# Optimization experiments

Hardware: AMD Instinct MI355X
Metric: run time of the kernel (lower is better)

Reference implementation:

```python
import jax, jax.numpy as jnp
import numpy as np

N_HEAD, D_MODEL, D_K, D_V = 16, 1024, 64, 64
BIAS_WEIGHT = 1.0
NEG = -10000.0


def setup_inputs() -> dict:
    key = jax.random.key(0)
    ks = jax.random.split(key, 9)
    B, L = 2, 2048
    q = jax.random.normal(ks[0], (B, L, D_MODEL), dtype=jnp.float32)
    k = jax.random.normal(ks[1], (B, L, D_MODEL), dtype=jnp.float32)
    v = jax.random.normal(ks[2], (B, L, D_MODEL), dtype=jnp.float32)
    mask = jax.random.randint(ks[3], (B, L, L), 0, 2, dtype=jnp.int32)
    bias = jax.random.normal(ks[4], (B, L, L), dtype=jnp.float32)
    s = 1.0 / np.sqrt(D_MODEL)
    w_qs = jax.random.uniform(ks[5], (D_MODEL, N_HEAD * D_K), jnp.float32, -s, s)
    w_ks = jax.random.uniform(ks[6], (D_MODEL, N_HEAD * D_K), jnp.float32, -s, s)
    w_vs = jax.random.uniform(ks[7], (D_MODEL, N_HEAD * D_V), jnp.float32, -s, s)
    w_fc = jax.random.uniform(ks[8], (N_HEAD * D_V, D_MODEL), jnp.float32, -s, s)
    return {"q": q, "k": k, "v": v, "mask": mask, "bias": bias,
            "w_qs": w_qs, "w_ks": w_ks, "w_vs": w_vs, "w_fc": w_fc}


def reference(q, k, v, mask, bias, w_qs, w_ks, w_vs, w_fc):
    B, Lq, _ = q.shape
    # project and split heads: [B, H, L, d]
    qh = (q @ w_qs).reshape(B, Lq, N_HEAD, D_K).transpose(0, 2, 1, 3)
    kh = (k @ w_ks).reshape(B, k.shape[1], N_HEAD, D_K).transpose(0, 2, 1, 3)
    vh = (v @ w_vs).reshape(B, v.shape[1], N_HEAD, D_V).transpose(0, 2, 1, 3)
    temperature = D_K ** 0.5
    attn = jnp.einsum('bhqd,bhkd->bhqk', qh / temperature, kh)
    attn = attn + bias[:, None, :, :] * BIAS_WEIGHT
    attn = jnp.where(mask[:, None, :, :] == 0, NEG, attn)
    attn = jax.nn.softmax(attn, axis=-1)
    out = jnp.einsum('bhqk,bhkd->bhqd', attn, vh)
    out = out.transpose(0, 2, 1, 3).reshape(B, Lq, N_HEAD * D_V)
    return out @ w_fc
```

## Files before the change

### kernel.cpp

```cpp
#include <hip/hip_runtime.h>
#include <cstddef>

#define DEV static __device__ __forceinline__

typedef float f32x4 __attribute__((ext_vector_type(4)));
typedef __bf16 bf16x8 __attribute__((ext_vector_type(8)));
typedef __bf16 bf16x4v __attribute__((ext_vector_type(4)));
typedef unsigned short u16x8 __attribute__((ext_vector_type(8)));
typedef unsigned short u16x4 __attribute__((ext_vector_type(4)));
typedef unsigned u32x2 __attribute__((ext_vector_type(2)));
typedef unsigned u32x4 __attribute__((ext_vector_type(4)));
typedef _Float16 f16;
typedef _Float16 f16x4 __attribute__((ext_vector_type(4)));

constexpr int BB = 2, LL = 2048, DM = 1024, NH = 16, DK = 64;
constexpr float LOG2E = 1.44269504f;

DEV unsigned short f2bf(float f) {
  unsigned u = __builtin_bit_cast(unsigned, f);
  u += 0x7fffu + ((u >> 16) & 1u);
  return (unsigned short)(u >> 16);
}
DEV u16x4 cvt4(f32x4 v) {
  bf16x4v b = __builtin_convertvector(v, bf16x4v);
  return __builtin_bit_cast(u16x4, b);
}
DEV bf16x8 asbf(u16x8 v) { return __builtin_bit_cast(bf16x8, v); }
DEV f32x4 mfma16(u16x8 a, u16x8 b, f32x4 c) {
  return __builtin_amdgcn_mfma_f32_16x16x32_bf16(asbf(a), asbf(b), c, 0, 0, 0);
}
#if __has_builtin(__builtin_amdgcn_exp2f)
DEV float fexp2(float x) { return __builtin_amdgcn_exp2f(x); }
#else
DEV float fexp2(float x) { return exp2f(x); }
#endif
DEV void swap32(unsigned& a, unsigned& b) {
#if __has_builtin(__builtin_amdgcn_permlane32_swap)
  u32x2 r = __builtin_amdgcn_permlane32_swap(a, b, false, false);
  a = r[0]; b = r[1];
#else
  asm("v_permlane32_swap_b32 %0, %1" : "+v"(a), "+v"(b));
#endif
}
DEV void swap16(unsigned& a, unsigned& b) {
#if __has_builtin(__builtin_amdgcn_permlane16_swap)
  u32x2 r = __builtin_amdgcn_permlane16_swap(a, b, false, false);
  a = r[0]; b = r[1];
#else
  asm("v_permlane16_swap_b32 %0, %1" : "+v"(a), "+v"(b));
#endif
}
DEV void g2lds16(const void* g, void* l) {
  __builtin_amdgcn_global_load_lds(
      (const __attribute__((address_space(1))) unsigned int*)g,
      (__attribute__((address_space(3))) unsigned int*)l, 16, 0, 0);
}

__global__ __launch_bounds__(256) void prep_all(
    const float* __restrict__ w0, const float* __restrict__ w1,
    const float* __restrict__ w2, const float* __restrict__ w3,
    unsigned short* __restrict__ wT, const float* __restrict__ s0,
    const float* __restrict__ s1, const float* __restrict__ s2,
    unsigned short* __restrict__ qkvb) {
  int f = blockIdx.x, t = threadIdx.x;
  if (f < 4096) {
    __shared__ float tile[32][33];
    int z = f >> 10, rem = f & 1023;
    int k0 = (rem >> 5) * 32, n0 = (rem & 31) * 32;
    const float* W = (z == 0) ? w0 : (z == 1) ? w1 : (z == 2) ? w2 : w3;
    unsigned short* out = wT + (size_t)z * DM * DM;
    int tx = t & 31, ty = t >> 5;
#pragma unroll
    for (int p = 0; p < 4; p++)
      tile[ty + 8 * p][tx] = W[(size_t)(k0 + ty + 8 * p) * DM + n0 + tx];
    __syncthreads();
#pragma unroll
    for (int p = 0; p < 4; p++)
      out[(size_t)(n0 + ty + 8 * p) * DM + k0 + tx] = f2bf(tile[tx][ty + 8 * p]);
  } else {
    int f3 = f - 4096;
    int z = f3 >> 11;
    const float* src = (z == 0) ? s0 : (z == 1) ? s1 : s2;
    size_t i = ((size_t)(f3 & 2047) * 256 + t) * 8;
    float4 a = *(const float4*)(src + i);
    float4 b = *(const float4*)(src + i + 4);
    u16x8 o;
    o[0] = f2bf(a.x); o[1] = f2bf(a.y); o[2] = f2bf(a.z); o[3] = f2bf(a.w);
    o[4] = f2bf(b.x); o[5] = f2bf(b.y); o[6] = f2bf(b.z); o[7] = f2bf(b.w);
    *(u16x8*)(qkvb + (size_t)z * (size_t)(BB * LL) * DM + i) = o;
  }
}

template <int KITERS>
DEV void gemm_core(const unsigned short* __restrict__ A,
                   const unsigned short* __restrict__ BT,
                   unsigned short* Al, unsigned short* Bl,
                   int m0, int n0, int k0beg, int t, f32x4 (&acc)[4][4]) {
  int lane = t & 63, c = lane & 15, qd = lane >> 4;
  int w = t >> 6, wm = w >> 1, wn = w & 1;
  int r0 = t >> 3;
  int gsw = (t & 7) ^ (r0 & 7);

#pragma unroll 1
  for (int kk = 0; kk < KITERS; ++kk) {
    int k0 = k0beg + kk * 64;
#pragma unroll
    for (int p = 0; p < 4; ++p) {
      g2lds16(&A[(size_t)(m0 + 32 * p + r0) * DM + k0 + 8 * gsw],
              &Al[p * 2048 + w * 512]);
      g2lds16(&BT[(size_t)(n0 + 32 * p + r0) * DM + k0 + 8 * gsw],
              &Bl[p * 2048 + w * 512]);
    }
    __syncthreads();
#pragma unroll
    for (int ks = 0; ks < 2; ++ks) {
      u16x8 af[4], bfr[4];
#pragma unroll
      for (int mt = 0; mt < 4; ++mt)
        af[mt] = *(const u16x8*)&Al[(64 * wm + 16 * mt + c) * 64 +
                                    (((4 * ks + qd) ^ (c & 7)) << 3)];
#pragma unroll
      for (int nt = 0; nt < 4; ++nt)
        bfr[nt] = *(const u16x8*)&Bl[(64 * wn + 16 * nt + c) * 64 +
                                     (((4 * ks + qd) ^ (c & 7)) << 3)];
#pragma unroll
      for (int mt = 0; mt < 4; ++mt)
#pragma unroll
        for (int nt = 0; nt < 4; ++nt)
          acc[mt][nt] = mfma16(af[mt], bfr[nt], acc[mt][nt]);
    }
    __syncthreads();
  }
}

__global__ __launch_bounds__(256, 3) void proj_gemm(
    const unsigned short* __restrict__ qkvb, const unsigned short* __restrict__ wT,
    unsigned short* __restrict__ qh, unsigned short* __restrict__ kh,
    unsigned short* __restrict__ vT, const int* __restrict__ mask,
    const float* __restrict__ bias, f16* __restrict__ bmf) {
  __shared__ unsigned short Al[128 * 64];
  __shared__ unsigned short Bl[128 * 64];
  int o = blockIdx.x, t = threadIdx.x;
  if (o >= 768) {
    int f2 = o - 768;
    int w = t >> 6, lane = t & 63;
    int bq = f2 >> 5;
    int kt = (f2 & 31) * 4 + w;
    int b = bq >> 7, qt = bq & 127;
    int q = qt * 16 + (lane & 15);
    int k = kt * 16 + (lane >> 4) * 4;
    size_t src = ((size_t)b * LL + q) * LL + k;
    int4 mk = *(const int4*)(mask + src);
    float4 bs = *(const float4*)(bias + src);
    f16x4 oo;
    oo[0] = (f16)((mk.x == 0 ? -10000.f : bs.x) * LOG2E);
    oo[1] = (f16)((mk.y == 0 ? -10000.f : bs.y) * LOG2E);
    oo[2] = (f16)((mk.z == 0 ? -10000.f : bs.z) * LOG2E);
    oo[3] = (f16)((mk.w == 0 ? -10000.f : bs.w) * LOG2E);
    *(f16x4*)(bmf + ((size_t)bq * 128 + kt) * 256 + lane * 4) = oo;
    return;
  }
  int wg = (o & 7) * 96 + (o >> 3);
  int z = wg >> 8, rem = wg & 255;
  int m0 = (rem >> 3) * 128, n0 = (rem & 7) * 128;
  const unsigned short* A = qkvb + (size_t)z * BB * LL * DM;
  const unsigned short* BT = wT + (size_t)z * DM * DM;
  int lane = t & 63, c = lane & 15, qd = lane >> 4;
  int w = t >> 6, wm = w >> 1, wn = w & 1;
  f32x4 acc[4][4] = {};
  gemm_core<DM / 64>(A, BT, Al, Bl, m0, n0, 0, t, acc);

  if (z == 2) {
#pragma unroll
    for (int mt = 0; mt < 4; ++mt)
#pragma unroll
      for (int nt = 0; nt < 4; ++nt) {
        int n = n0 + 64 * wn + 16 * nt + c;
        int h = n >> 6, d = n & 63;
        int m = m0 + 64 * wm + 16 * mt + 4 * qd;
        int b = m >> 11, l = m & 2047;
        *(u16x4*)&vT[(((size_t)b * NH + h) * DK + d) * LL + l] = cvt4(acc[mt][nt]);
      }
  } else {
    unsigned short* Ch = z ? kh : qh;
    float scale = z ? 1.0f : 0.125f * LOG2E;
#pragma unroll
    for (int mt = 0; mt < 4; ++mt)
#pragma unroll
      for (int nt = 0; nt < 4; ++nt) {
        int n = n0 + 64 * wn + 16 * nt + c;
        int h = n >> 6, d = n & 63;
#pragma unroll
        for (int i = 0; i < 4; ++i) {
          int m = m0 + 64 * wm + 16 * mt + 4 * qd + i;
          int b = m >> 11, l = m & 2047;
          Ch[(((size_t)b * NH + h) * LL + l) * DK + d] = f2bf(acc[mt][nt][i] * scale);
        }
      }
  }
}

__global__ __launch_bounds__(256, 2) void fc_gemm(const unsigned short* __restrict__ A,
                                                  const unsigned short* __restrict__ BT,
                                                  float* __restrict__ C) {
  __shared__ unsigned short Al[64 * 64];
  __shared__ unsigned short Bl[128 * 64];
  int o = blockIdx.x;
  int wg = (o & 7) * 64 + (o >> 3);
  int m0 = (wg >> 3) * 64, n0 = (wg & 7) * 128;
  int t = threadIdx.x, lane = t & 63, c = lane & 15, qd = lane >> 4;
  int w = t >> 6, wm = w >> 1, wn = w & 1;
  int r0 = t >> 3, gsw = (t & 7) ^ (r0 & 7);
  f32x4 acc[2][4] = {};

#pragma unroll 1
  for (int kk = 0; kk < 16; ++kk) {
    int k0 = kk * 64;
#pragma unroll
    for (int p = 0; p < 2; ++p)
      g2lds16(&A[(size_t)(m0 + 32 * p + r0) * DM + k0 + 8 * gsw],
              &Al[p * 2048 + w * 512]);
#pragma unroll
    for (int p = 0; p < 4; ++p)
      g2lds16(&BT[(size_t)(n0 + 32 * p + r0) * DM + k0 + 8 * gsw],
              &Bl[p * 2048 + w * 512]);
    __syncthreads();
#pragma unroll
    for (int ks = 0; ks < 2; ++ks) {
      u16x8 af[2], bfr[4];
#pragma unroll
      for (int mt = 0; mt < 2; ++mt)
        af[mt] = *(const u16x8*)&Al[(32 * wm + 16 * mt + c) * 64 +
                                    (((4 * ks + qd) ^ (c & 7)) << 3)];
#pragma unroll
      for (int nt = 0; nt < 4; ++nt)
        bfr[nt] = *(const u16x8*)&Bl[(64 * wn + 16 * nt + c) * 64 +
                                     (((4 * ks + qd) ^ (c & 7)) << 3)];
#pragma unroll
      for (int mt = 0; mt < 2; ++mt)
#pragma unroll
        for (int nt = 0; nt < 4; ++nt)
          acc[mt][nt] = mfma16(af[mt], bfr[nt], acc[mt][nt]);
    }
    __syncthreads();
  }

#pragma unroll
  for (int mt = 0; mt < 2; ++mt)
#pragma unroll
    for (int nt = 0; nt < 4; ++nt) {
      int n = n0 + 64 * wn + 16 * nt + c;
#pragma unroll
      for (int i = 0; i < 4; ++i) {
        int m = m0 + 32 * wm + 16 * mt + 4 * qd + i;
        C[(size_t)m * DM + n] = acc[mt][nt][i];
      }
    }
}

__global__ __launch_bounds__(256, 4) void attn_kern(
    const unsigned short* __restrict__ qh, const unsigned short* __restrict__ kh,
    const unsigned short* __restrict__ vT, const f16* __restrict__ bmf,
    unsigned short* __restrict__ O) {
  __shared__ unsigned short Kb[2][4096];
  __shared__ unsigned short Vb[3][4096];

  int t = threadIdx.x, w = t >> 6, lane = t & 63, c = lane & 15, qd = lane >> 4;
  int o = blockIdx.x;
  int wg = (o & 7) * 128 + (o >> 3);
  int x = wg & 31, h = (wg >> 5) & 15, b = wg >> 9;
  int q0 = x * 64;
  const unsigned short* Q = qh + (((size_t)b * NH + h) * LL + q0) * DK;
  const unsigned short* K = kh + ((size_t)b * NH + h) * LL * DK;
  const unsigned short* V = vT + ((size_t)b * NH + h) * DK * LL;
  const f16* BMF = bmf + (((size_t)b * 128 + x * 4 + w) * 128) * 256 + lane * 4;
  int rt = t >> 3, gg = t & 7;

  f16x4 bc[4], bn[4];
#pragma unroll
  for (int r = 0; r < 2; ++r) {
    int row = r * 32 + rt;
    int sc = ((gg ^ (row & 7)) << 3);
    g2lds16(&Q[(size_t)row * DK + sc], &Kb[1][r * 2048 + w * 512]);
    g2lds16(&K[(size_t)row * DK + sc], &Kb[0][r * 2048 + w * 512]);
    g2lds16(&V[(size_t)row * LL + sc], &Vb[0][r * 2048 + w * 512]);
  }
#pragma unroll
  for (int mt = 0; mt < 4; ++mt) bc[mt] = *(const f16x4*)&BMF[(size_t)mt * 256];
  __syncthreads();

  u16x8 qf[2];
#pragma unroll
  for (int ks = 0; ks < 2; ++ks)
    qf[ks] = *(const u16x8*)&Kb[1][(16 * w + c) * 64 +
                                   (((4 * ks + qd) ^ (c & 7)) << 3)];
  __syncthreads();

  {
#pragma unroll
    for (int r = 0; r < 2; ++r) {
      int row = r * 32 + rt;
      int sc = ((gg ^ (row & 7)) << 3);
      g2lds16(&K[(size_t)(64 + row) * DK + sc], &Kb[1][r * 2048 + w * 512]);
      g2lds16(&V[(size_t)row * LL + 64 + sc], &Vb[1][r * 2048 + w * 512]);
    }
#pragma unroll
    for (int mt = 0; mt < 4; ++mt)
      bn[mt] = *(const f16x4*)&BMF[(size_t)(4 + mt) * 256];
  }
  f32x4 sP[4];
  __builtin_amdgcn_s_setprio(1);
#pragma unroll
  for (int mt = 0; mt < 4; ++mt) {
    int row = 16 * mt + c;
    u16x8 k0f = *(const u16x8*)&Kb[0][row * 64 + ((qd ^ (c & 7)) << 3)];
    u16x8 k1f = *(const u16x8*)&Kb[0][row * 64 + (((4 + qd) ^ (c & 7)) << 3)];
    f16x4 b4 = bc[mt];
    f32x4 z = {(float)b4[0], (float)b4[1], (float)b4[2], (float)b4[3]};
    z = mfma16(k0f, qf[0], z);
    sP[mt] = mfma16(k1f, qf[1], z);
  }
  __builtin_amdgcn_s_setprio(0);
#pragma unroll
  for (int mt = 0; mt < 4; ++mt) bc[mt] = bn[mt];
  __syncthreads();

  const u16x8 ones = {0x3F80, 0x3F80, 0x3F80, 0x3F80,
                      0x3F80, 0x3F80, 0x3F80, 0x3F80};
  f32x4 lacc = {};
  f32x4 oacc[4] = {};
  unsigned short* Vr = Vb[0];
  unsigned short* Vc = Vb[1];
  unsigned short* Vw = Vb[2];

#pragma unroll 1
  for (int j = 1; j < 32; ++j) {
    const unsigned short* Kl = Kb[j & 1];
    unsigned short* Kw = Kb[(j + 1) & 1];
    if (j + 1 < 32) {
      int kt1 = (j + 1) * 64;
#pragma unroll
      for (int r = 0; r < 2; ++r) {
        int row = r * 32 + rt;
        int sc = ((gg ^ (row & 7)) << 3);
        g2lds16(&K[(size_t)(kt1 + row) * DK + sc], &Kw[r * 2048 + w * 512]);
        g2lds16(&V[(size_t)row * LL + kt1 + sc], &Vw[r * 2048 + w * 512]);
      }
#pragma unroll
      for (int mt = 0; mt < 4; ++mt)
        bn[mt] = *(const f16x4*)&BMF[(size_t)((j + 1) * 4 + mt) * 256];
    }

    __builtin_amdgcn_s_setprio(1);
    u16x8 pf[2];
    {
      unsigned L[4], H[4];
#pragma unroll
      for (int mt = 0; mt < 4; ++mt) {
        f32x4 p;
#pragma unroll
        for (int i = 0; i < 4; ++i) p[i] = fexp2(sP[mt][i]);
        u32x2 lw = __builtin_bit_cast(u32x2, cvt4(p));
        L[mt] = lw[0];
        H[mt] = lw[1];
      }
#pragma unroll
      for (int ks = 0; ks < 2; ++ks) {
        unsigned l0 = L[2 * ks], l1 = L[2 * ks + 1];
        unsigned h0 = H[2 * ks], h1 = H[2 * ks + 1];
        swap32(l0, l1); swap16(l0, l1);
        swap32(h0, h1); swap16(h0, h1);
        u32x4 pw = {l0, h0, l1, h1};
        pf[ks] = __builtin_bit_cast(u16x8, pw);
      }
    }
    f32x4 sN[4];
#pragma unroll
    for (int mt = 0; mt < 4; ++mt) {
      int row = 16 * mt + c;
      u16x8 k0f = *(const u16x8*)&Kl[row * 64 + ((qd ^ (c & 7)) << 3)];
      u16x8 k1f = *(const u16x8*)&Kl[row * 64 + (((4 + qd) ^ (c & 7)) << 3)];
      f16x4 b4 = bc[mt];
      f32x4 z = {(float)b4[0], (float)b4[1], (float)b4[2], (float)b4[3]};
      z = mfma16(k0f, qf[0], z);
      sN[mt] = mfma16(k1f, qf[1], z);
    }
    lacc = mfma16(ones, pf[0], lacc);
    lacc = mfma16(ones, pf[1], lacc);
#pragma unroll
    for (int dt = 0; dt < 4; ++dt) {
      int row = 16 * dt + c;
      u16x8 v0f = *(const u16x8*)&Vr[row * 64 + ((qd ^ (c & 7)) << 3)];
      u16x8 v1f = *(const u16x8*)&Vr[row * 64 + (((4 + qd) ^ (c & 7)) << 3)];
      oacc[dt] = mfma16(v0f, pf[0], oacc[dt]);
      oacc[dt] = mfma16(v1f, pf[1], oacc[dt]);
    }
    __builtin_amdgcn_s_setprio(0);

#pragma unroll
    for (int mt = 0; mt < 4; ++mt) { sP[mt] = sN[mt]; bc[mt] = bn[mt]; }
    unsigned short* tv = Vr; Vr = Vc; Vc = Vw; Vw = tv;
    __syncthreads();
  }

  {
    u16x8 pf[2];
    unsigned L[4], H[4];
#pragma unroll
    for (int mt = 0; mt < 4; ++mt) {
      f32x4 p;
#pragma unroll
      for (int i = 0; i < 4; ++i) p[i] = fexp2(sP[mt][i]);
      u32x2 lw = __builtin_bit_cast(u32x2, cvt4(p));
      L[mt] = lw[0]; H[mt] = lw[1];
    }
#pragma unroll
    for (int ks = 0; ks < 2; ++ks) {
      unsigned l0 = L[2 * ks], l1 = L[2 * ks + 1];
      unsigned h0 = H[2 * ks], h1 = H[2 * ks + 1];
      swap32(l0, l1); swap16(l0, l1);
      swap32(h0, h1); swap16(h0, h1);
      u32x4 pw = {l0, h0, l1, h1};
      pf[ks] = __builtin_bit_cast(u16x8, pw);
    }
    lacc = mfma16(ones, pf[0], lacc);
    lacc = mfma16(ones, pf[1], lacc);
#pragma unroll
    for (int dt = 0; dt < 4; ++dt) {
      int row = 16 * dt + c;
      u16x8 v0f = *(const u16x8*)&Vr[row * 64 + ((qd ^ (c & 7)) << 3)];
      u16x8 v1f = *(const u16x8*)&Vr[row * 64 + (((4 + qd) ^ (c & 7)) << 3)];
      oacc[dt] = mfma16(v0f, pf[0], oacc[dt]);
      oacc[dt] = mfma16(v1f, pf[1], oacc[dt]);
    }
  }

  {
    float rl = 1.f / lacc[0];
    size_t orow = ((size_t)b * LL + q0 + 16 * w + c) * DM + h * DK;
#pragma unroll
    for (int dt = 0; dt < 4; ++dt)
      *(u16x4*)&O[orow + 16 * dt + 4 * qd] = cvt4(oacc[dt] * rl);
  }
}

extern "C" void kernel_launch(void* const* d_in, const int* in_sizes, int n_in,
                              void* d_out, int out_size, void* d_ws, size_t ws_size,
                              hipStream_t stream) {
  (void)in_sizes; (void)n_in; (void)ws_size; (void)out_size;
  const float* q = (const float*)d_in[0];
  const float* k = (const float*)d_in[1];
  const float* v = (const float*)d_in[2];
  const int* mask = (const int*)d_in[3];
  const float* bias = (const float*)d_in[4];
  const float* w_qs = (const float*)d_in[5];
  const float* w_ks = (const float*)d_in[6];
  const float* w_vs = (const float*)d_in[7];
  const float* w_fc = (const float*)d_in[8];

  char* ws = (char*)d_ws;
  const size_t MB = 1024 * 1024;
  unsigned short* wT = (unsigned short*)(ws);
  f16* bmf = (f16*)(ws + 8 * MB);
  unsigned short* qkvb = (unsigned short*)(ws + 24 * MB);
  unsigned short* qh = (unsigned short*)(ws + 48 * MB);
  unsigned short* kh = (unsigned short*)(ws + 56 * MB);
  unsigned short* vhT = (unsigned short*)(ws + 64 * MB);
  unsigned short* Obuf = (unsigned short*)(ws + 72 * MB);

  prep_all<<<dim3(10240), dim3(256), 0, stream>>>(w_qs, w_ks, w_vs, w_fc, wT,
                                                  q, k, v, qkvb);
  proj_gemm<<<dim3(8960), 256, 0, stream>>>(qkvb, wT, qh, kh, vhT, mask, bias,
                                            bmf);
  attn_kern<<<dim3(1024), dim3(256), 0, stream>>>(qh, kh, vhT, bmf, Obuf);
  fc_gemm<<<dim3(512), 256, 0, stream>>>(Obuf, wT + (size_t)3 * DM * DM,
                                         (float*)d_out);
}
```

Before: 256.2 us.

## Fuse fp32-to-bf16 input conversion into projection GEMM A-tile loads

Removes the separate pass that converted q/k/v to bf16 and instead loads fp32 activations directly in the projection GEMM, converting to bf16 before storing into shared memory. This eliminates one full read/write pass over the activations and a workspace buffer. In exchange the GEMM reads twice as many bytes for A per tile and uses synchronous register loads instead of async global-to-LDS copies, which may reduce latency hiding.

```diff
diff --git a/kernel.cpp b/kernel.cpp
--- a/kernel.cpp
+++ b/kernel.cpp
@@ -59,36 +59,21 @@
 __global__ __launch_bounds__(256) void prep_all(
     const float* __restrict__ w0, const float* __restrict__ w1,
     const float* __restrict__ w2, const float* __restrict__ w3,
-    unsigned short* __restrict__ wT, const float* __restrict__ s0,
-    const float* __restrict__ s1, const float* __restrict__ s2,
-    unsigned short* __restrict__ qkvb) {
+    unsigned short* __restrict__ wT) {
   int f = blockIdx.x, t = threadIdx.x;
-  if (f < 4096) {
-    __shared__ float tile[32][33];
-    int z = f >> 10, rem = f & 1023;
-    int k0 = (rem >> 5) * 32, n0 = (rem & 31) * 32;
-    const float* W = (z == 0) ? w0 : (z == 1) ? w1 : (z == 2) ? w2 : w3;
-    unsigned short* out = wT + (size_t)z * DM * DM;
-    int tx = t & 31, ty = t >> 5;
-#pragma unroll
-    for (int p = 0; p < 4; p++)
-      tile[ty + 8 * p][tx] = W[(size_t)(k0 + ty + 8 * p) * DM + n0 + tx];
-    __syncthreads();
-#pragma unroll
-    for (int p = 0; p < 4; p++)
-      out[(size_t)(n0 + ty + 8 * p) * DM + k0 + tx] = f2bf(tile[tx][ty + 8 * p]);
-  } else {
-    int f3 = f - 4096;
-    int z = f3 >> 11;
-    const float* src = (z == 0) ? s0 : (z == 1) ? s1 : s2;
-    size_t i = ((size_t)(f3 & 2047) * 256 + t) * 8;
-    float4 a = *(const float4*)(src + i);
-    float4 b = *(const float4*)(src + i + 4);
-    u16x8 o;
-    o[0] = f2bf(a.x); o[1] = f2bf(a.y); o[2] = f2bf(a.z); o[3] = f2bf(a.w);
-    o[4] = f2bf(b.x); o[5] = f2bf(b.y); o[6] = f2bf(b.z); o[7] = f2bf(b.w);
-    *(u16x8*)(qkvb + (size_t)z * (size_t)(BB * LL) * DM + i) = o;
-  }
+  __shared__ float tile[32][33];
+  int z = f >> 10, rem = f & 1023;
+  int k0 = (rem >> 5) * 32, n0 = (rem & 31) * 32;
+  const float* W = (z == 0) ? w0 : (z == 1) ? w1 : (z == 2) ? w2 : w3;
+  unsigned short* out = wT + (size_t)z * DM * DM;
+  int tx = t & 31, ty = t >> 5;
+#pragma unroll
+  for (int p = 0; p < 4; p++)
+    tile[ty + 8 * p][tx] = W[(size_t)(k0 + ty + 8 * p) * DM + n0 + tx];
+  __syncthreads();
+#pragma unroll
+  for (int p = 0; p < 4; p++)
+    out[(size_t)(n0 + ty + 8 * p) * DM + k0 + tx] = f2bf(tile[tx][ty + 8 * p]);
 }
 
 template <int KITERS>
@@ -133,8 +118,62 @@
   }
 }
 
+template <int KITERS>
+DEV void gemm_core_f32a(const float* __restrict__ A,
+                        const unsigned short* __restrict__ BT,
+                        unsigned short* Al, unsigned short* Bl,
+                        int m0, int n0, int t, f32x4 (&acc)[4][4]) {
+  int lane = t & 63, c = lane & 15, qd = lane >> 4;
+  int w = t >> 6, wm = w >> 1, wn = w & 1;
+  int r0 = t >> 3;
+  int gsw = (t & 7) ^ (r0 & 7);
+
+#pragma unroll 1
+  for (int kk = 0; kk < KITERS; ++kk) {
+    int k0 = kk * 64;
+    float4 a0[4], a1[4];
+#pragma unroll
+    for (int p = 0; p < 4; ++p) {
+      const float* ap = &A[(size_t)(m0 + 32 * p + r0) * DM + k0 + 8 * gsw];
+      a0[p] = *(const float4*)ap;
+      a1[p] = *(const float4*)(ap + 4);
+      g2lds16(&BT[(size_t)(n0 + 32 * p + r0) * DM + k0 + 8 * gsw],
+              &Bl[p * 2048 + w * 512]);
+    }
+#pragma unroll
+    for (int p = 0; p < 4; ++p) {
+      u16x8 o;
+      o[0] = f2bf(a0[p].x); o[1] = f2bf(a0[p].y);
+      o[2] = f2bf(a0[p].z); o[3] = f2bf(a0[p].w);
+      o[4] = f2bf(a1[p].x); o[5] = f2bf(a1[p].y);
+      o[6] = f2bf(a1[p].z); o[7] = f2bf(a1[p].w);
+      *(u16x8*)&Al[p * 2048 + t * 8] = o;
+    }
+    __syncthreads();
+#pragma unroll
+    for (int ks = 0; ks < 2; ++ks) {
+      u16x8 af[4], bfr[4];
+#pragma unroll
+      for (int mt = 0; mt < 4; ++mt)
+        af[mt] = *(const u16x8*)&Al[(64 * wm + 16 * mt + c) * 64 +
+                                    (((4 * ks + qd) ^ (c & 7)) << 3)];
+#pragma unroll
+      for (int nt = 0; nt < 4; ++nt)
+        bfr[nt] = *(const u16x8*)&Bl[(64 * wn + 16 * nt + c) * 64 +
+                                     (((4 * ks + qd) ^ (c & 7)) << 3)];
+#pragma unroll
+      for (int mt = 0; mt < 4; ++mt)
+#pragma unroll
+        for (int nt = 0; nt < 4; ++nt)
+          acc[mt][nt] = mfma16(af[mt], bfr[nt], acc[mt][nt]);
+    }
+    __syncthreads();
+  }
+}
+
 __global__ __launch_bounds__(256, 3) void proj_gemm(
-    const unsigned short* __restrict__ qkvb, const unsigned short* __restrict__ wT,
+    const float* __restrict__ qf32, const float* __restrict__ kf32,
+    const float* __restrict__ vf32, const unsigned short* __restrict__ wT,
     unsigned short* __restrict__ qh, unsigned short* __restrict__ kh,
     unsigned short* __restrict__ vT, const int* __restrict__ mask,
     const float* __restrict__ bias, f16* __restrict__ bmf) {
@@ -163,12 +202,12 @@
   int wg = (o & 7) * 96 + (o >> 3);
   int z = wg >> 8, rem = wg & 255;
   int m0 = (rem >> 3) * 128, n0 = (rem & 7) * 128;
-  const unsigned short* A = qkvb + (size_t)z * BB * LL * DM;
+  const float* A = (z == 0) ? qf32 : (z == 1) ? kf32 : vf32;
   const unsigned short* BT = wT + (size_t)z * DM * DM;
   int lane = t & 63, c = lane & 15, qd = lane >> 4;
   int w = t >> 6, wm = w >> 1, wn = w & 1;
   f32x4 acc[4][4] = {};
-  gemm_core<DM / 64>(A, BT, Al, Bl, m0, n0, 0, t, acc);
+  gemm_core_f32a<DM / 64>(A, BT, Al, Bl, m0, n0, t, acc);
 
   if (z == 2) {
 #pragma unroll
@@ -462,16 +501,14 @@
   const size_t MB = 1024 * 1024;
   unsigned short* wT = (unsigned short*)(ws);
   f16* bmf = (f16*)(ws + 8 * MB);
-  unsigned short* qkvb = (unsigned short*)(ws + 24 * MB);
   unsigned short* qh = (unsigned short*)(ws + 48 * MB);
   unsigned short* kh = (unsigned short*)(ws + 56 * MB);
   unsigned short* vhT = (unsigned short*)(ws + 64 * MB);
   unsigned short* Obuf = (unsigned short*)(ws + 72 * MB);
 
-  prep_all<<<dim3(10240), dim3(256), 0, stream>>>(w_qs, w_ks, w_vs, w_fc, wT,
-                                                  q, k, v, qkvb);
-  proj_gemm<<<dim3(8960), 256, 0, stream>>>(qkvb, wT, qh, kh, vhT, mask, bias,
-                                            bmf);
+  prep_all<<<dim3(4096), dim3(256), 0, stream>>>(w_qs, w_ks, w_vs, w_fc, wT);
+  proj_gemm<<<dim3(8960), 256, 0, stream>>>(q, k, v, wT, qh, kh, vhT, mask,
+                                            bias, bmf);
   attn_kern<<<dim3(1024), dim3(256), 0, stream>>>(qh, kh, vhT, bmf, Obuf);
   fc_gemm<<<dim3(512), 256, 0, stream>>>(Obuf, wT + (size_t)3 * DM * DM,
                                          (float*)d_out);
```

After: 262.5 us. +2.4%, slower.
